# Performance work log

Hardware: AMD Instinct MI355X
Metric: run time of the kernel (lower is better)

## Reference

```python
import jax, jax.numpy as jnp
import numpy as np

B, T, L, V = 2048, 256, 32, 128
BLANK = V - 1          # Keras/TF CTC uses last class as blank
EPS = 1e-7             # keras backend epsilon used in ctc_batch_cost's log
NEG = -1e30            # log-space -inf surrogate (fp-safe)


def setup_inputs() -> dict:
    key = jax.random.key(0)
    k1, k2 = jax.random.split(key)
    # y_pred are softmax posteriors, as ctc_batch_cost expects
    logits = jax.random.normal(k1, (B, T, V), dtype=jnp.float32)
    y_pred = jax.nn.softmax(logits, axis=-1)
    # labels exclude the blank class (V-1)
    y_true = jax.random.randint(k2, (B, L), 0, BLANK, dtype=jnp.int64)
    return {"y_true": y_true, "y_pred": y_pred}


def _ctc_loss(y_true, y_pred):
    Bb, Tt, Vv = y_pred.shape
    Ll = y_true.shape[1]
    S = 2 * Ll + 1  # extended label length: blank-interleaved

    # extended labels: [blank, l1, blank, l2, ..., lL, blank]  -> [B, S]
    ext = jnp.full((Bb, S), BLANK, dtype=y_true.dtype).at[:, 1::2].set(y_true)

    logp = jnp.log(y_pred + EPS)  # [B, T, V], matches K.ctc_batch_cost
    # gather per-frame log-probs of each extended-label symbol: [B, T, S]
    lp_ext = jnp.take_along_axis(
        logp, jnp.broadcast_to(ext[:, None, :], (Bb, Tt, S)), axis=2
    )

    # skip transition (s-2 -> s) allowed iff ext[s] != blank and ext[s] != ext[s-2]
    ext_m2 = jnp.pad(ext, ((0, 0), (2, 0)), constant_values=-1)[:, :S]
    skip = (ext != BLANK) & (ext != ext_m2)  # [B, S]

    # alpha init at t=0: only first blank and first label reachable
    alpha0 = (
        jnp.full((Bb, S), NEG, dtype=logp.dtype)
        .at[:, 0].set(lp_ext[:, 0, 0])
        .at[:, 1].set(lp_ext[:, 0, 1])
    )

    def step(alpha, lp_t):
        # alpha: [B, S], lp_t: [B, S]
        s1 = jnp.pad(alpha, ((0, 0), (1, 0)), constant_values=NEG)[:, :S]
        s2 = jnp.pad(alpha, ((0, 0), (2, 0)), constant_values=NEG)[:, :S]
        a = jnp.logaddexp(alpha, s1)
        a = jnp.logaddexp(a, jnp.where(skip, s2, NEG))
        return a + lp_t, None

    lp_ts = jnp.transpose(lp_ext, (1, 0, 2))[1:]  # [T-1, B, S]
    alphaT, _ = jax.lax.scan(step, alpha0, lp_ts)

    # total log-likelihood = logsumexp over last blank and last label states
    loss = -jnp.logaddexp(alphaT[:, S - 1], alphaT[:, S - 2])  # [B]
    return loss[:, None]  # K.ctc_batch_cost returns [B, 1]


def reference(y_true, y_pred):
    return _ctc_loss(y_true, y_pred)
```

## Files before the change

### kernel.cpp

```cpp
#include <hip/hip_runtime.h>


constexpr int Bb = 2048;
constexpr int Tt = 256;
constexpr int Ll = 32;
constexpr int Vv = 128;
constexpr int BLANK = Vv - 1;
constexpr int CHUNK = 16;
constexpr int NCH = Tt / CHUNK;
#define EPSF 1e-7f
#define NEGF -1e30f
#define LN2F 0.6931471805599453f

__device__ __forceinline__ float fexp2(float x) { return __builtin_amdgcn_exp2f(x); }
__device__ __forceinline__ float flog2(float x) { return __builtin_amdgcn_logf(x); }
__device__ __forceinline__ float rdlane(float v, int l) {
    return __uint_as_float(__builtin_amdgcn_readlane(__float_as_uint(v), l));
}
__device__ __forceinline__ float dpp_shr1(float old, float src) {
    return __int_as_float(__builtin_amdgcn_update_dpp(
        __float_as_int(old), __float_as_int(src), 0x138 ,
        0xf, 0xf, false));
}

__global__ __launch_bounds__(128) void ctc_fwd(const int* __restrict__ y_true,
                                               const float* __restrict__ y_pred,
                                               float* __restrict__ out) {
    const int w    = blockIdx.x;
    const int wave = threadIdx.x >> 6;
    const int lane = threadIdx.x & 63;

    __shared__ float buf[2][CHUNK][64];

    int sym = BLANK;
    if (!(lane & 1)) sym = y_true[w * Ll + (lane >> 1)];

    if (wave == 0) {
        const float* rp = y_pred + (size_t)w * Tt * Vv + sym;
        float rA[CHUNK], rB[CHUNK];
#pragma unroll
        for (int i = 0; i < CHUNK; ++i) rA[i] = rp[(size_t)i * Vv];
        for (int cc = 0; cc < NCH / 2; ++cc) {
            const int c0 = 2 * cc, c1 = 2 * cc + 1;
#pragma unroll
            for (int i = 0; i < CHUNK; ++i)
                rB[i] = rp[(size_t)(c1 * CHUNK + i) * Vv];
#pragma unroll
            for (int i = 0; i < CHUNK; ++i)
                buf[0][i][lane] = flog2(rA[i] + EPSF);
            __syncthreads();
            if (c1 + 1 < NCH) {
#pragma unroll
                for (int i = 0; i < CHUNK; ++i)
                    rA[i] = rp[(size_t)((c1 + 1) * CHUNK + i) * Vv];
            }
#pragma unroll
            for (int i = 0; i < CHUNK; ++i)
                buf[1][i][lane] = flog2(rB[i] + EPSF);
            __syncthreads();
        }
    } else {
        const int  symm2 = __shfl_up(sym, 2);
        const bool skip  = !(lane & 1) && (lane >= 2) && (sym != symm2);

        float m = NEGF, p = 1.0f, b0 = 0.0f;

        auto step = [&](float lp2) {
            const float lpb = rdlane(lp2, 1);
            const float b0p = b0;
            const float m1g = dpp_shr1(b0p,  m);
            const float p1g = dpp_shr1(1.0f, p);
            const float m2s = dpp_shr1(NEGF, m1g);
            const float p2g = dpp_shr1(1.0f, p1g);
            const float m2g = skip ? m2s : NEGF;
            const float hi  = fmaxf(fmaxf(m, m1g), m2g);
            const float pn  = p   * fexp2(m   - hi)
                            + p1g * fexp2(m1g - hi)
                            + p2g * fexp2(m2g - hi);
            m  = hi + lp2;
            p  = pn;
            b0 = b0p + lpb;
        };
        auto renorm = [&]() {
            m += flog2(fmaxf(p, 1e-30f));  p = 1.0f;
        };

        for (int c = 0; c < NCH; ++c) {
            __syncthreads();
            float lp[CHUNK];
#pragma unroll
            for (int i = 0; i < CHUNK; ++i) lp[i] = buf[c & 1][i][lane];
            if (c == 0) {
                b0 = rdlane(lp[0], 1);
                m  = (lane == 0) ? lp[0] : NEGF;
                p  = 1.0f;
#pragma unroll
                for (int i = 1; i < CHUNK; ++i) {
                    step(lp[i]);
                    if ((i & 7) == 7) renorm();
                }
            } else {
#pragma unroll
                for (int i = 0; i < CHUNK; ++i) {
                    step(lp[i]);
                    if ((i & 7) == 7) renorm();
                }
            }
        }

        const float afin = m + flog2(fmaxf(p, 1e-30f));
        const float aA = rdlane(afin, 62);
        const float aB = rdlane(afin, 63);
        if (lane == 0) {
            const float h = fmaxf(aA, aB);
            const float r = h + flog2(fexp2(aA - h) + fexp2(aB - h));
            out[w] = -r * LN2F;
        }
    }
}

extern "C" void kernel_launch(void* const* d_in, const int* in_sizes, int n_in,
                              void* d_out, int out_size, void* d_ws, size_t ws_size,
                              hipStream_t stream) {
    const int*   y_true = (const int*)d_in[0];
    const float* y_pred = (const float*)d_in[1];
    float*       out    = (float*)d_out;
    ctc_fwd<<<dim3(Bb), dim3(128), 0, stream>>>(y_true, y_pred, out);
}
```

Measured before the change: 46.66 us.

## Stream full probability chunks into LDS with direct global-to-LDS loads

The producer wave now copies whole contiguous CHUNK x V slabs of y_pred into a triple-buffered LDS ring using global_load_lds, waiting on vmcnt, instead of issuing strided per-symbol register loads. The compute wave gathers its symbol from LDS and applies the log itself. This swaps scattered 4-byte global reads for coalesced 16-byte DMA-style transfers, but moves 8x more bytes from global memory than the per-symbol gather. It also puts the log on the serial recurrence wave and raises LDS use per block.

```diff
diff --git a/kernel.cpp b/kernel.cpp
--- a/kernel.cpp
+++ b/kernel.cpp
@@ -11,6 +11,9 @@
 #define EPSF 1e-7f
 #define NEGF -1e30f
 #define LN2F 0.6931471805599453f
+
+#define GLOBAL_AS(p) ((const __attribute__((address_space(1))) void*)(p))
+#define LDS_AS(p)    ((__attribute__((address_space(3))) void*)(p))
 
 __device__ __forceinline__ float fexp2(float x) { return __builtin_amdgcn_exp2f(x); }
 __device__ __forceinline__ float flog2(float x) { return __builtin_amdgcn_logf(x); }
@@ -30,36 +33,31 @@
     const int wave = threadIdx.x >> 6;
     const int lane = threadIdx.x & 63;
 
-    __shared__ float buf[2][CHUNK][64];
-
-    int sym = BLANK;
-    if (!(lane & 1)) sym = y_true[w * Ll + (lane >> 1)];
+    __shared__ float buf[3][CHUNK * Vv];
 
     if (wave == 0) {
-        const float* rp = y_pred + (size_t)w * Tt * Vv + sym;
-        float rA[CHUNK], rB[CHUNK];
+        const float* gbase = y_pred + (size_t)w * Tt * Vv;
+        auto issue = [&](int c, float* dst) {
+            const float* g = gbase + (size_t)c * (CHUNK * Vv) + lane * 4;
+            float*       l = dst + lane * 4;
 #pragma unroll
-        for (int i = 0; i < CHUNK; ++i) rA[i] = rp[(size_t)i * Vv];
-        for (int cc = 0; cc < NCH / 2; ++cc) {
-            const int c0 = 2 * cc, c1 = 2 * cc + 1;
-#pragma unroll
-            for (int i = 0; i < CHUNK; ++i)
-                rB[i] = rp[(size_t)(c1 * CHUNK + i) * Vv];
-#pragma unroll
-            for (int i = 0; i < CHUNK; ++i)
-                buf[0][i][lane] = flog2(rA[i] + EPSF);
-            __syncthreads();
-            if (c1 + 1 < NCH) {
-#pragma unroll
-                for (int i = 0; i < CHUNK; ++i)
-                    rA[i] = rp[(size_t)((c1 + 1) * CHUNK + i) * Vv];
+            for (int i = 0; i < 8; ++i)
+                __builtin_amdgcn_global_load_lds(GLOBAL_AS(g + i * 256),
+                                                 LDS_AS(l + i * 256), 16, 0, 0);
+        };
+        issue(0, buf[0]);
+        for (int c = 0; c < NCH; ++c) {
+            if (c + 1 < NCH) {
+                issue(c + 1, buf[(c + 1) % 3]);
+                asm volatile("s_waitcnt vmcnt(8)" ::: "memory");
+            } else {
+                asm volatile("s_waitcnt vmcnt(0)" ::: "memory");
             }
-#pragma unroll
-            for (int i = 0; i < CHUNK; ++i)
-                buf[1][i][lane] = flog2(rB[i] + EPSF);
             __syncthreads();
         }
     } else {
+        int sym = BLANK;
+        if (!(lane & 1)) sym = y_true[w * Ll + (lane >> 1)];
         const int  symm2 = __shfl_up(sym, 2);
         const bool skip  = !(lane & 1) && (lane >= 2) && (sym != symm2);
 
@@ -87,9 +85,11 @@
 
         for (int c = 0; c < NCH; ++c) {
             __syncthreads();
+            const float* src = buf[c % 3];
             float lp[CHUNK];
 #pragma unroll
-            for (int i = 0; i < CHUNK; ++i) lp[i] = buf[c & 1][i][lane];
+            for (int i = 0; i < CHUNK; ++i)
+                lp[i] = flog2(src[i * Vv + sym] + EPSF);
             if (c == 0) {
                 b0 = rdlane(lp[0], 1);
                 m  = (lane == 0) ? lp[0] : NEGF;
```

Result: slower. 62.85 us (+34.7%).

## Use three producer waves round-robin with four-slot LDS ring for log-prob staging

Applied to the files above, without the earlier changes.

Replaces the single producer wave with three producer waves that take chunks in round-robin order. Each producer keeps a load up to three chunks ahead, and the LDS buffer grows to four slots. The goal is more global loads in flight, so the consumer wave running the serial alpha recursion spends less time waiting at the barriers. In exchange the block grows to 256 threads, mostly idle producer waves now hit every barrier, and fewer blocks may fit per CU.

```diff
diff --git a/kernel.cpp b/kernel.cpp
--- a/kernel.cpp
+++ b/kernel.cpp
@@ -8,6 +8,7 @@
 constexpr int BLANK = Vv - 1;
 constexpr int CHUNK = 16;
 constexpr int NCH = Tt / CHUNK;
+constexpr int SLOTS = 4;
 #define EPSF 1e-7f
 #define NEGF -1e30f
 #define LN2F 0.6931471805599453f
@@ -23,41 +24,36 @@
         0xf, 0xf, false));
 }
 
-__global__ __launch_bounds__(128) void ctc_fwd(const int* __restrict__ y_true,
+__global__ __launch_bounds__(256) void ctc_fwd(const int* __restrict__ y_true,
                                                const float* __restrict__ y_pred,
                                                float* __restrict__ out) {
     const int w    = blockIdx.x;
     const int wave = threadIdx.x >> 6;
     const int lane = threadIdx.x & 63;
 
-    __shared__ float buf[2][CHUNK][64];
+    __shared__ float buf[SLOTS][CHUNK][64];
 
     int sym = BLANK;
     if (!(lane & 1)) sym = y_true[w * Ll + (lane >> 1)];
 
-    if (wave == 0) {
+    if (wave >= 1) {
+        const int p = wave - 1;
         const float* rp = y_pred + (size_t)w * Tt * Vv + sym;
-        float rA[CHUNK], rB[CHUNK];
+        float r[CHUNK];
 #pragma unroll
-        for (int i = 0; i < CHUNK; ++i) rA[i] = rp[(size_t)i * Vv];
-        for (int cc = 0; cc < NCH / 2; ++cc) {
-            const int c0 = 2 * cc, c1 = 2 * cc + 1;
-#pragma unroll
-            for (int i = 0; i < CHUNK; ++i)
-                rB[i] = rp[(size_t)(c1 * CHUNK + i) * Vv];
-#pragma unroll
-            for (int i = 0; i < CHUNK; ++i)
-                buf[0][i][lane] = flog2(rA[i] + EPSF);
-            __syncthreads();
-            if (c1 + 1 < NCH) {
+        for (int i = 0; i < CHUNK; ++i) r[i] = rp[(size_t)(p * CHUNK + i) * Vv];
+        for (int c = 0; c < NCH; ++c) {
+            if (c % 3 == p) {
 #pragma unroll
                 for (int i = 0; i < CHUNK; ++i)
-                    rA[i] = rp[(size_t)((c1 + 1) * CHUNK + i) * Vv];
+                    buf[c & (SLOTS - 1)][i][lane] = flog2(r[i] + EPSF);
             }
+            __syncthreads();
+            if (c % 3 == p && c + 3 < NCH) {
 #pragma unroll
-            for (int i = 0; i < CHUNK; ++i)
-                buf[1][i][lane] = flog2(rB[i] + EPSF);
-            __syncthreads();
+                for (int i = 0; i < CHUNK; ++i)
+                    r[i] = rp[(size_t)((c + 3) * CHUNK + i) * Vv];
+            }
         }
     } else {
         const int  symm2 = __shfl_up(sym, 2);
@@ -89,7 +85,7 @@
             __syncthreads();
             float lp[CHUNK];
 #pragma unroll
-            for (int i = 0; i < CHUNK; ++i) lp[i] = buf[c & 1][i][lane];
+            for (int i = 0; i < CHUNK; ++i) lp[i] = buf[c & (SLOTS - 1)][i][lane];
             if (c == 0) {
                 b0 = rdlane(lp[0], 1);
                 m  = (lane == 0) ? lp[0] : NEGF;
@@ -125,5 +121,5 @@
     const int*   y_true = (const int*)d_in[0];
     const float* y_pred = (const float*)d_in[1];
     float*       out    = (float*)d_out;
-    ctc_fwd<<<dim3(Bb), dim3(128), 0, stream>>>(y_true, y_pred, out);
+    ctc_fwd<<<dim3(Bb), dim3(256), 0, stream>>>(y_true, y_pred, out);
 }
```

Result: slower. 49.70 us (+6.5%).
